# Kernel tuning notes

Hardware: AMD Instinct MI355X
Metric: run time of the kernel (lower is better)

The kernel has to match this reference:

```python
import jax, jax.numpy as jnp
import numpy as np

B, T, D, H, C = 128, 1024, 256, 256, 128


def setup_inputs() -> dict:
    key = jax.random.key(0)
    ks = jax.random.split(key, 10)
    s = 0.02  # scale down randn init so sigmoid/tanh don't saturate numerically
    inp = {
        "x": jax.random.normal(ks[0], (B, T, D), dtype=jnp.float32),
        "W_xi": jax.random.normal(ks[1], (D, H), dtype=jnp.float32) * s,
        "W_hi": jax.random.normal(ks[2], (H, H), dtype=jnp.float32) * s,
        "b_i": jnp.zeros((H,), jnp.float32),
        "W_xf": jax.random.normal(ks[3], (D, H), dtype=jnp.float32) * s,
        "W_hf": jax.random.normal(ks[4], (H, H), dtype=jnp.float32) * s,
        "b_f": jnp.zeros((H,), jnp.float32),
        "W_xg": jax.random.normal(ks[5], (D, H), dtype=jnp.float32) * s,
        "W_hg": jax.random.normal(ks[6], (H, H), dtype=jnp.float32) * s,
        "b_g": jnp.zeros((H,), jnp.float32),
        "W_xo": jax.random.normal(ks[7], (D, H), dtype=jnp.float32) * s,
        "W_ho": jax.random.normal(ks[8], (H, H), dtype=jnp.float32) * s,
        "b_o": jnp.zeros((H,), jnp.float32),
        "W_hy": jax.random.normal(ks[9], (H, C), dtype=jnp.float32) * s,
        "b_y": jnp.zeros((C,), jnp.float32),
    }
    return inp


def reference(x, W_xi, W_hi, b_i, W_xf, W_hf, b_f, W_xg, W_hg, b_g,
              W_xo, W_ho, b_o, W_hy, b_y):
    batch, _, _ = x.shape
    hid = W_hi.shape[0]
    # Precompute all input projections for all timesteps (4 big GEMMs).
    xi = jnp.einsum("btd,dh->bth", x, W_xi) + b_i
    xf = jnp.einsum("btd,dh->bth", x, W_xf) + b_f
    xg = jnp.einsum("btd,dh->bth", x, W_xg) + b_g
    xo = jnp.einsum("btd,dh->bth", x, W_xo) + b_o
    # Time-major stacked gate pre-activations: [T, B, 4H]
    gates_x = jnp.concatenate([xi, xf, xg, xo], axis=-1).transpose(1, 0, 2)
    W_h = jnp.concatenate([W_hi, W_hf, W_hg, W_ho], axis=1)  # [H, 4H]

    def step(carry, gx_t):
        h, c = carry
        z = gx_t + h @ W_h  # [B, 4H]
        i_t = jax.nn.sigmoid(z[:, 0 * hid:1 * hid])
        f_t = jax.nn.sigmoid(z[:, 1 * hid:2 * hid])
        g_t = jnp.tanh(z[:, 2 * hid:3 * hid])
        o_t = jax.nn.sigmoid(z[:, 3 * hid:4 * hid])
        c_new = f_t * c + i_t * g_t
        h_new = o_t * jnp.tanh(c_new)
        return (h_new, c_new), None

    h0 = jnp.zeros((batch, hid), x.dtype)
    c0 = jnp.zeros((batch, hid), x.dtype)
    (h_T, _), _ = jax.lax.scan(step, (h0, c0), gates_x)
    return h_T @ W_hy + b_y
```

## Files before the change

### kernel.cpp

```cpp
#include <hip/hip_runtime.h>

using u16 = unsigned short;
using u32 = unsigned int;

typedef _Float16 f16x2 __attribute__((ext_vector_type(2)));
typedef _Float16 f16x8 __attribute__((ext_vector_type(8)));
typedef float    f32x4 __attribute__((ext_vector_type(4)));

__device__ __forceinline__ u16 f16bits(float x) {
  union { _Float16 h; u16 u; } r; r.h = (_Float16)x; return r.u;
}
__device__ __forceinline__ float h2f(u16 v) {
  union { u16 u; _Float16 h; } r; r.u = v; return (float)r.h;
}
__device__ __forceinline__ u32 pack2(float a, float b) {
  union { f16x2 h; u32 u; } r; r.h.x = (_Float16)a; r.h.y = (_Float16)b; return r.u;
}
__device__ __forceinline__ float fdot2a(u32 a, u32 b, float c) {
  union { u32 u; f16x2 h; } ua, ub; ua.u = a; ub.u = b;
#if __has_builtin(__builtin_amdgcn_fdot2)
  return __builtin_amdgcn_fdot2(ua.h, ub.h, c, false);
#else
  return c + (float)ua.h.x * (float)ub.h.x + (float)ua.h.y * (float)ub.h.y;
#endif
}
__device__ __forceinline__ float sigmoidf_(float x) { return 1.0f / (1.0f + __expf(-x)); }
__device__ __forceinline__ float tanhf_(float x)    { return 1.0f - 2.0f / (__expf(2.0f * x) + 1.0f); }

__device__ __forceinline__ f16x8 lds16(const u16* p) {
  union { uint4 u; f16x8 h; } r; r.u = *(const uint4*)p; return r.h;
}

__device__ __forceinline__ float qreduce(float a) {
#if __has_builtin(__builtin_amdgcn_permlane16_swap) && __has_builtin(__builtin_amdgcn_permlane32_swap)
  typedef unsigned uv2 __attribute__((ext_vector_type(2)));
  union { float f; unsigned u; } x, p, q;
  x.f = a;
  uv2 r1 = __builtin_amdgcn_permlane16_swap(x.u, x.u, false, false);
  p.u = r1[0]; q.u = r1[1];
  float s = p.f + q.f;
  x.f = s;
  uv2 r2 = __builtin_amdgcn_permlane32_swap(x.u, x.u, false, false);
  p.u = r2[0]; q.u = r2[1];
  return p.f + q.f;
#else
  a += __shfl_xor(a, 16);
  a += __shfl_xor(a, 32);
  return a;
#endif
}

__global__ void lstm_prep(const float* __restrict__ Wxi, const float* __restrict__ Wxf,
                          const float* __restrict__ Wxg, const float* __restrict__ Wxo,
                          const float* __restrict__ Whi, const float* __restrict__ Whf,
                          const float* __restrict__ Whg, const float* __restrict__ Who,
                          u16* __restrict__ WxT, u32* __restrict__ Whpp,
                          u32* __restrict__ h16s, float* __restrict__ c_s) {
  int idx = blockIdx.x * 256 + threadIdx.x;
  if (idx < 262144) {
    int n = idx >> 8, k = idx & 255;
    int g = n >> 8;
    const float* W = (g == 0) ? Wxi : (g == 1) ? Wxf : (g == 2) ? Wxg : Wxo;
    WxT[idx] = f16bits(W[k * 256 + (n & 255)]);
  } else if (idx < 262144 + 131072) {
    int i2 = idx - 262144;
    int e = i2 & 3, tmp = i2 >> 2;
    int t = tmp & 1023, i4 = tmp >> 10;
    int cc = i4 >> 3, pp = i4 & 7;
    int w = t >> 6, l = t & 63, q = l >> 4;
    int j = w * 64 + (l & 15) * 4 + cc;
    int kk = q * 32 + pp * 4 + e;
    int g = j >> 8, col = j & 255;
    const float* W = (g == 0) ? Whi : (g == 1) ? Whf : (g == 2) ? Whg : Who;
    u32 lo = f16bits(W[(2 * kk) * 256 + col]);
    u32 hi = f16bits(W[(2 * kk + 1) * 256 + col]);
    Whpp[i2] = lo | (hi << 16);
  } else if (idx < 262144 + 131072 + 16384) {
    h16s[idx - 393216] = 0u;
  } else if (idx < 262144 + 131072 + 16384 + 32768) {
    c_s[idx - 409600] = 0.0f;
  }
}

__global__ __launch_bounds__(256) void proj_gemm(
    const float* __restrict__ x, const u16* __restrict__ WxT,
    u16* __restrict__ gates, const float* __restrict__ bi,
    const float* __restrict__ bf, const float* __restrict__ bg,
    const float* __restrict__ bo, int t0, int tcShift) {
  __shared__ u16 Al[128 * 72];
  __shared__ u16 Bl[128 * 72];
  const int tid = threadIdx.x;
  const int lane = tid & 63, wv = tid >> 6;
  const int wr = wv >> 1, wc = wv & 1;
  const int m0 = blockIdx.x * 128, n0 = blockIdx.y * 128;
  const int tcMask = (1 << tcShift) - 1;
  f32x4 acc[4][4] = {};
  for (int k0 = 0; k0 < 256; k0 += 64) {
#pragma unroll
    for (int p = 0; p < 8; ++p) {
      int flat = p * 256 + tid;
      int r = flat >> 4, cc = flat & 15;
      int m = m0 + r;
      int b = m >> tcShift, tc = m & tcMask;
      const float4 xv = *(const float4*)(x + (size_t)(b * 1024 + t0 + tc) * 256 + k0 + cc * 4);
      uint2 w2 = make_uint2(pack2(xv.x, xv.y), pack2(xv.z, xv.w));
      *(uint2*)&Al[r * 72 + cc * 4] = w2;
    }
#pragma unroll
    for (int p = 0; p < 8; ++p) {
      int flat = p * 256 + tid;
      int r = flat >> 4, cc = flat & 15;
      uint2 w2 = *(const uint2*)(WxT + (size_t)(n0 + r) * 256 + k0 + cc * 4);
      *(uint2*)&Bl[r * 72 + cc * 4] = w2;
    }
    __syncthreads();
#pragma unroll
    for (int kk = 0; kk < 64; kk += 32) {
      f16x8 af[4], bfr[4];
#pragma unroll
      for (int i = 0; i < 4; ++i) {
        af[i]  = lds16(&Al[(wr * 64 + i * 16 + (lane & 15)) * 72 + kk + (lane >> 4) * 8]);
        bfr[i] = lds16(&Bl[(wc * 64 + i * 16 + (lane & 15)) * 72 + kk + (lane >> 4) * 8]);
      }
#pragma unroll
      for (int mi = 0; mi < 4; ++mi)
#pragma unroll
        for (int ni = 0; ni < 4; ++ni)
          acc[mi][ni] = __builtin_amdgcn_mfma_f32_16x16x32_f16(af[mi], bfr[ni], acc[mi][ni], 0, 0, 0);
    }
    __syncthreads();
  }
#pragma unroll
  for (int ni = 0; ni < 4; ++ni) {
    int n = n0 + wc * 64 + ni * 16 + (lane & 15);
    int g = n >> 8;
    const float* bp = (g == 0) ? bi : (g == 1) ? bf : (g == 2) ? bg : bo;
    float bias = bp[n & 255];
#pragma unroll
    for (int mi = 0; mi < 4; ++mi) {
#pragma unroll
      for (int ri = 0; ri < 4; ++ri) {
        int m = m0 + wr * 64 + mi * 16 + (lane >> 4) * 4 + ri;
        gates[(size_t)m * 1024 + n] = f16bits(acc[mi][ni][ri] + bias);
      }
    }
  }
}

__global__ __launch_bounds__(1024) void lstm_rec(
    const u32* __restrict__ Whpp, const u16* __restrict__ gates,
    u32* __restrict__ h16s, float* __restrict__ c_s,
    const float* __restrict__ Why, const float* __restrict__ by,
    float* __restrict__ out, int Tc, int last) {
  extern __shared__ unsigned char smem[];
  uint4* ldsW = (uint4*)smem;
  u32*   hq   = (u32*)(smem + 131072);
  float* zbuf = (float*)(smem + 131072 + 1280);
  const int b = blockIdx.x, t = threadIdx.x;
  const int l = t & 63, w = t >> 6, q = l >> 4;
  const int jb = w * 64 + (l & 15) * 4;

  u32 wreg[96];
  const uint4* Wp4 = (const uint4*)Whpp;
#pragma unroll
  for (int i4 = 0; i4 < 32; ++i4) {
    uint4 v = Wp4[i4 * 1024 + t];
    const int cc = i4 >> 3, pp = i4 & 7;
    if (pp < 6) {
      wreg[cc * 24 + pp * 4 + 0] = v.x;
      wreg[cc * 24 + pp * 4 + 1] = v.y;
      wreg[cc * 24 + pp * 4 + 2] = v.z;
      wreg[cc * 24 + pp * 4 + 3] = v.w;
    } else {
      ldsW[(cc * 2 + (pp - 6)) * 1024 + t] = v;
    }
  }
  if (t < 128) hq[(t >> 5) * 40 + (t & 31)] = h16s[b * 128 + t];
  float c = 0.0f;
  if (t < 256) c = c_s[b * 256 + t];
  const u16* gxp = gates + (size_t)b * Tc * 1024 + jb;
  uint2 pre = *(const uint2*)gxp;
  int buf = 0;
  const int evenWave = ((w & 1) == 0);
  __syncthreads();

#define REGDOTS                                                         \
  _Pragma("unroll")                                                     \
  for (int pp = 0; pp < 6; ++pp) {                                      \
    uint4 hv = hb[pp];                                                  \
    _Pragma("unroll")                                                   \
    for (int cc = 0; cc < 4; ++cc) {                                    \
      acc[cc] = fdot2a(hv.x, wreg[cc * 24 + pp * 4 + 0], acc[cc]);      \
      acc[cc] = fdot2a(hv.y, wreg[cc * 24 + pp * 4 + 1], acc[cc]);      \
      acc[cc] = fdot2a(hv.z, wreg[cc * 24 + pp * 4 + 2], acc[cc]);      \
      acc[cc] = fdot2a(hv.w, wreg[cc * 24 + pp * 4 + 3], acc[cc]);      \
    }                                                                   \
  }
#define LDSDOTS                                                         \
  _Pragma("unroll")                                                     \
  for (int pp = 6; pp < 8; ++pp) {                                      \
    uint4 hv = hb[pp];                                                  \
    _Pragma("unroll")                                                   \
    for (int cc = 0; cc < 4; ++cc) {                                    \
      uint4 wv = ldsW[(cc * 2 + (pp - 6)) * 1024 + t];                  \
      acc[cc] = fdot2a(hv.x, wv.x, acc[cc]);                            \
      acc[cc] = fdot2a(hv.y, wv.y, acc[cc]);                            \
      acc[cc] = fdot2a(hv.z, wv.z, acc[cc]);                            \
      acc[cc] = fdot2a(hv.w, wv.w, acc[cc]);                            \
    }                                                                   \
  }

  for (int tc = 0; tc < Tc; ++tc) {
    const uint2 gx = pre;
    if (tc + 1 < Tc) pre = *(const uint2*)(gxp + (size_t)(tc + 1) * 1024);
    float acc[4] = {0.f, 0.f, 0.f, 0.f};
    const uint4* hb = (const uint4*)(hq + buf * 160 + q * 40);
    __builtin_amdgcn_s_setprio(1);
    if (evenWave) {
      REGDOTS
      LDSDOTS
    } else {
      LDSDOTS
      REGDOTS
    }
    __builtin_amdgcn_s_setprio(0);
    acc[0] = qreduce(acc[0]);
    acc[1] = qreduce(acc[1]);
    acc[2] = qreduce(acc[2]);
    acc[3] = qreduce(acc[3]);
    if (l < 16) {
      float4 z4;
      z4.x = acc[0] + h2f((u16)(gx.x & 0xffff));
      z4.y = acc[1] + h2f((u16)(gx.x >> 16));
      z4.z = acc[2] + h2f((u16)(gx.y & 0xffff));
      z4.w = acc[3] + h2f((u16)(gx.y >> 16));
      *(float4*)&zbuf[jb] = z4;
    }
    __syncthreads();
    if (t < 256) {
      float zi = zbuf[t], zf = zbuf[t + 256], zg = zbuf[t + 512], zo = zbuf[t + 768];
      float i_ = sigmoidf_(zi), f_ = sigmoidf_(zf), g_ = tanhf_(zg), o_ = sigmoidf_(zo);
      c = f_ * c + i_ * g_;
      float h_ = o_ * tanhf_(c);
      const int kk = t >> 1;
      ((u16*)(hq + (buf ^ 1) * 160))[((kk >> 5) * 40 + (kk & 31)) * 2 + (t & 1)] = f16bits(h_);
    }
    buf ^= 1;
    __syncthreads();
  }
#undef REGDOTS
#undef LDSDOTS

  if (t < 128) h16s[b * 128 + t] = hq[buf * 160 + (t >> 5) * 40 + (t & 31)];
  if (t < 256) c_s[b * 256 + t] = c;

  if (last && t < 128) {
    float acc = by[t];
    const u16* hh = (const u16*)(hq + buf * 160);
#pragma unroll 8
    for (int k = 0; k < 256; ++k) {
      float hv = h2f(hh[((k >> 6) * 40 + ((k >> 1) & 31)) * 2 + (k & 1)]);
      acc += hv * Why[k * 128 + t];
    }
    out[b * 128 + t] = acc;
  }
}

extern "C" void kernel_launch(void* const* d_in, const int* in_sizes, int n_in,
                              void* d_out, int out_size, void* d_ws, size_t ws_size,
                              hipStream_t stream) {
  const float* x   = (const float*)d_in[0];
  const float* Wxi = (const float*)d_in[1];
  const float* Whi = (const float*)d_in[2];
  const float* b_i = (const float*)d_in[3];
  const float* Wxf = (const float*)d_in[4];
  const float* Whf = (const float*)d_in[5];
  const float* b_f = (const float*)d_in[6];
  const float* Wxg = (const float*)d_in[7];
  const float* Whg = (const float*)d_in[8];
  const float* b_g = (const float*)d_in[9];
  const float* Wxo = (const float*)d_in[10];
  const float* Who = (const float*)d_in[11];
  const float* b_o = (const float*)d_in[12];
  const float* Why = (const float*)d_in[13];
  const float* b_y = (const float*)d_in[14];
  float* out = (float*)d_out;

  int Tc = 256;
  while (Tc > 32 && (size_t)128 * Tc * 1024 * 2 + 1245184ull > ws_size) Tc >>= 1;
  const int tcShift = __builtin_ctz((unsigned)Tc);
  const int nch = 1024 / Tc;

  char* wsb = (char*)d_ws;
  const size_t gbytes = (size_t)128 * Tc * 1024 * 2;
  u16*   gates16 = (u16*)wsb;
  u16*   WxT     = (u16*)(wsb + gbytes);
  u32*   Whpp    = (u32*)(wsb + gbytes + 524288);
  u32*   h16s    = (u32*)(wsb + gbytes + 1048576);
  float* c_s     = (float*)(wsb + gbytes + 1048576 + 65536);

  const int recLds = 131072 + 1280 + 4096;
  (void)hipFuncSetAttribute((const void*)lstm_rec,
                            hipFuncAttributeMaxDynamicSharedMemorySize, recLds);

  lstm_prep<<<1728, 256, 0, stream>>>(Wxi, Wxf, Wxg, Wxo, Whi, Whf, Whg, Who,
                                      WxT, Whpp, h16s, c_s);
  for (int ci = 0; ci < nch; ++ci) {
    int t0 = ci * Tc;
    proj_gemm<<<dim3(Tc, 8), 256, 0, stream>>>(x, WxT, gates16, b_i, b_f, b_g, b_o,
                                               t0, tcShift);
    lstm_rec<<<128, 1024, recLds, stream>>>(Whpp, gates16, h16s, c_s, Why, b_y, out,
                                            Tc, (ci == nch - 1) ? 1 : 0);
  }
}
```

Before: 1.854 ms.

## Halve recurrent block to 512 threads with eight gate columns per thread

Result: slower. 1.969 ms (+6.2%).

```diff
diff --git a/kernel.cpp b/kernel.cpp
--- a/kernel.cpp
+++ b/kernel.cpp
@@ -65,10 +65,10 @@
   } else if (idx < 262144 + 131072) {
     int i2 = idx - 262144;
     int e = i2 & 3, tmp = i2 >> 2;
-    int t = tmp & 1023, i4 = tmp >> 10;
+    int t = tmp & 511, i4 = tmp >> 9;
     int cc = i4 >> 3, pp = i4 & 7;
     int w = t >> 6, l = t & 63, q = l >> 4;
-    int j = w * 64 + (l & 15) * 4 + cc;
+    int j = w * 128 + (l & 15) * 8 + cc;
     int kk = q * 32 + pp * 4 + e;
     int g = j >> 8, col = j & 255;
     const float* W = (g == 0) ? Whi : (g == 1) ? Whf : (g == 2) ? Whg : Who;
@@ -147,7 +147,7 @@
   }
 }
 
-__global__ __launch_bounds__(1024) void lstm_rec(
+__global__ __launch_bounds__(512, 2) void lstm_rec(
     const u32* __restrict__ Whpp, const u16* __restrict__ gates,
     u32* __restrict__ h16s, float* __restrict__ c_s,
     const float* __restrict__ Why, const float* __restrict__ by,
@@ -158,13 +158,13 @@
   float* zbuf = (float*)(smem + 131072 + 1280);
   const int b = blockIdx.x, t = threadIdx.x;
   const int l = t & 63, w = t >> 6, q = l >> 4;
-  const int jb = w * 64 + (l & 15) * 4;
-
-  u32 wreg[96];
+  const int jb = w * 128 + (l & 15) * 8;
+
+  u32 wreg[192];
   const uint4* Wp4 = (const uint4*)Whpp;
 #pragma unroll
-  for (int i4 = 0; i4 < 32; ++i4) {
-    uint4 v = Wp4[i4 * 1024 + t];
+  for (int i4 = 0; i4 < 64; ++i4) {
+    uint4 v = Wp4[i4 * 512 + t];
     const int cc = i4 >> 3, pp = i4 & 7;
     if (pp < 6) {
       wreg[cc * 24 + pp * 4 + 0] = v.x;
@@ -172,14 +172,14 @@
       wreg[cc * 24 + pp * 4 + 2] = v.z;
       wreg[cc * 24 + pp * 4 + 3] = v.w;
     } else {
-      ldsW[(cc * 2 + (pp - 6)) * 1024 + t] = v;
+      ldsW[(cc * 2 + (pp - 6)) * 512 + t] = v;
     }
   }
   if (t < 128) hq[(t >> 5) * 40 + (t & 31)] = h16s[b * 128 + t];
   float c = 0.0f;
   if (t < 256) c = c_s[b * 256 + t];
   const u16* gxp = gates + (size_t)b * Tc * 1024 + jb;
-  uint2 pre = *(const uint2*)gxp;
+  uint4 pre = *(const uint4*)gxp;
   int buf = 0;
   const int evenWave = ((w & 1) == 0);
   __syncthreads();
@@ -189,7 +189,7 @@
   for (int pp = 0; pp < 6; ++pp) {                                      \
     uint4 hv = hb[pp];                                                  \
     _Pragma("unroll")                                                   \
-    for (int cc = 0; cc < 4; ++cc) {                                    \
+    for (int cc = 0; cc < 8; ++cc) {                                    \
       acc[cc] = fdot2a(hv.x, wreg[cc * 24 + pp * 4 + 0], acc[cc]);      \
       acc[cc] = fdot2a(hv.y, wreg[cc * 24 + pp * 4 + 1], acc[cc]);      \
       acc[cc] = fdot2a(hv.z, wreg[cc * 24 + pp * 4 + 2], acc[cc]);      \
@@ -201,8 +201,8 @@
   for (int pp = 6; pp < 8; ++pp) {                                      \
     uint4 hv = hb[pp];                                                  \
     _Pragma("unroll")                                                   \
-    for (int cc = 0; cc < 4; ++cc) {                                    \
-      uint4 wv = ldsW[(cc * 2 + (pp - 6)) * 1024 + t];                  \
+    for (int cc = 0; cc < 8; ++cc) {                                    \
+      uint4 wv = ldsW[(cc * 2 + (pp - 6)) * 512 + t];                   \
       acc[cc] = fdot2a(hv.x, wv.x, acc[cc]);                            \
       acc[cc] = fdot2a(hv.y, wv.y, acc[cc]);                            \
       acc[cc] = fdot2a(hv.z, wv.z, acc[cc]);                            \
@@ -211,9 +211,9 @@
   }
 
   for (int tc = 0; tc < Tc; ++tc) {
-    const uint2 gx = pre;
-    if (tc + 1 < Tc) pre = *(const uint2*)(gxp + (size_t)(tc + 1) * 1024);
-    float acc[4] = {0.f, 0.f, 0.f, 0.f};
+    const uint4 gx = pre;
+    if (tc + 1 < Tc) pre = *(const uint4*)(gxp + (size_t)(tc + 1) * 1024);
+    float acc[8] = {0.f, 0.f, 0.f, 0.f, 0.f, 0.f, 0.f, 0.f};
     const uint4* hb = (const uint4*)(hq + buf * 160 + q * 40);
     __builtin_amdgcn_s_setprio(1);
     if (evenWave) {
@@ -224,17 +224,20 @@
       REGDOTS
     }
     __builtin_amdgcn_s_setprio(0);
-    acc[0] = qreduce(acc[0]);
-    acc[1] = qreduce(acc[1]);
-    acc[2] = qreduce(acc[2]);
-    acc[3] = qreduce(acc[3]);
+#pragma unroll
+    for (int i = 0; i < 8; ++i) acc[i] = qreduce(acc[i]);
     if (l < 16) {
-      float4 z4;
-      z4.x = acc[0] + h2f((u16)(gx.x & 0xffff));
-      z4.y = acc[1] + h2f((u16)(gx.x >> 16));
-      z4.z = acc[2] + h2f((u16)(gx.y & 0xffff));
-      z4.w = acc[3] + h2f((u16)(gx.y >> 16));
-      *(float4*)&zbuf[jb] = z4;
+      float4 z4a, z4b;
+      z4a.x = acc[0] + h2f((u16)(gx.x & 0xffff));
+      z4a.y = acc[1] + h2f((u16)(gx.x >> 16));
+      z4a.z = acc[2] + h2f((u16)(gx.y & 0xffff));
+      z4a.w = acc[3] + h2f((u16)(gx.y >> 16));
+      z4b.x = acc[4] + h2f((u16)(gx.z & 0xffff));
+      z4b.y = acc[5] + h2f((u16)(gx.z >> 16));
+      z4b.z = acc[6] + h2f((u16)(gx.w & 0xffff));
+      z4b.w = acc[7] + h2f((u16)(gx.w >> 16));
+      *(float4*)&zbuf[jb] = z4a;
+      *(float4*)&zbuf[jb + 4] = z4b;
     }
     __syncthreads();
     if (t < 256) {
@@ -309,7 +312,7 @@
     int t0 = ci * Tc;
     proj_gemm<<<dim3(Tc, 8), 256, 0, stream>>>(x, WxT, gates16, b_i, b_f, b_g, b_o,
                                                t0, tcShift);
-    lstm_rec<<<128, 1024, recLds, stream>>>(Whpp, gates16, h16s, c_s, Why, b_y, out,
-                                            Tc, (ci == nch - 1) ? 1 : 0);
-  }
-}
+    lstm_rec<<<128, 512, recLds, stream>>>(Whpp, gates16, h16s, c_s, Why, b_y, out,
+                                           Tc, (ci == nch - 1) ? 1 : 0);
+  }
+}
```
